# Optimization experiments

Measured on AMD Instinct MI355X. Metric: run time of the kernel, lower is better.

The kernel has to match this reference:

```python
import jax, jax.numpy as jnp
import numpy as np

T, B, DIN, DH, NH = 256, 256, 1024, 1024, 16
HD = DH // NH


def setup_inputs() -> dict:
    key = jax.random.key(0)
    ks = jax.random.split(key, 11)
    w = lambda k, shape: jax.random.normal(k, shape, jnp.float32) * 0.02
    return {
        "inputs": jax.random.normal(ks[0], (T, B, DIN), jnp.float32),
        "Wg": w(ks[1], (4, DIN + DH, DH)),  # forget, input, update, output pre-gate linears
        "bg": w(ks[2], (4, DH)),
        "Wq": w(ks[3], (3, DH, DH)),  # forget, input, output attention gates
        "bq": w(ks[4], (3, DH)),
        "Wk": w(ks[5], (3, DH, DH)),
        "bk": w(ks[6], (3, DH)),
        "Wv": w(ks[7], (3, DH, DH)),
        "bv": w(ks[8], (3, DH)),
        "Wo": w(ks[9], (3, DH, DH)),
        "bo": w(ks[10], (3, DH)),
    }


def reference(inputs, Wg, bg, Wq, bq, Wk, bk, Wv, bv, Wo, bo):
    scale = 1.0 / np.sqrt(HD)
    sel = jnp.array([0, 1, 3])  # gates that use attention: forget, input, output

    def attn_gate(x):
        # x: [3, B, DH] -- three gate pre-activations processed in parallel
        q = (jnp.einsum('gbd,gde->gbe', x, Wq) + bq[:, None, :]).reshape(3, B, NH, HD)
        k = (jnp.einsum('gbd,gde->gbe', x, Wk) + bk[:, None, :]).reshape(3, B, NH, HD)
        v = (jnp.einsum('gbd,gde->gbe', x, Wv) + bv[:, None, :]).reshape(3, B, NH, HD)
        # attention ACROSS heads: [3, B, NH, NH]
        aw = jax.nn.softmax(jnp.einsum('gbhd,gbkd->gbhk', q, k) * scale, axis=-1)
        ao = jnp.einsum('gbhk,gbkd->gbhd', aw, v).reshape(3, B, DH)
        return jax.nn.sigmoid(jnp.einsum('gbd,gde->gbe', ao, Wo) + bo[:, None, :])

    def step(carry, x):
        hx, cx = carry
        comb = jnp.concatenate([x, hx], axis=1)          # [B, DIN+DH]
        pre = jnp.einsum('bi,gio->gbo', comb, Wg) + bg[:, None, :]  # [4, B, DH]
        f, i, o = attn_gate(pre[sel])                    # each [B, DH]
        g = jnp.tanh(pre[2])
        cx = f * cx + i * g
        hx = o * jnp.tanh(cx)
        return (hx, cx), hx

    init = (jnp.zeros((B, DH), inputs.dtype), jnp.zeros((B, DH), inputs.dtype))
    (hx, cx), outputs = jax.lax.scan(step, init, inputs)
    return outputs, hx, cx
```

## Files before the change

kernel.cpp:

```cpp
#include <hip/hip_runtime.h>

typedef __attribute__((ext_vector_type(8))) short bf8;
typedef __attribute__((ext_vector_type(8))) unsigned short us8;
typedef __attribute__((ext_vector_type(4))) unsigned short us4;
typedef __attribute__((ext_vector_type(4))) float f4;

#define NB 256
#define OUT_HX_OFF ((size_t)256 * 256 * 1024)
#define OUT_CX_OFF (OUT_HX_OFF + (size_t)256 * 1024)

static __device__ __forceinline__ unsigned short f2bf(float f) {
    unsigned u = __builtin_bit_cast(unsigned, f);
    return (unsigned short)((u + 0x7FFFu + ((u >> 16) & 1u)) >> 16);
}
static __device__ __forceinline__ float bf2f(unsigned short h) {
    return __builtin_bit_cast(float, (unsigned)h << 16);
}
static __device__ __forceinline__ float sigm(float x) {
    return 1.0f / (1.0f + __expf(-x));
}

#define MFMA16(a, b, c) __builtin_amdgcn_mfma_f32_16x16x32_bf16(a, b, c, 0, 0, 0)

#define GLDS16(g, l)                                                        \
    __builtin_amdgcn_global_load_lds(                                       \
        (const __attribute__((address_space(1))) void*)(g),                 \
        (__attribute__((address_space(3))) void*)(l), 16, 0, 0)

#define WAITV(n) asm volatile("s_waitcnt vmcnt(" #n ")" ::: "memory")
#define WAITL0 asm volatile("s_waitcnt lgkmcnt(0)" ::: "memory")
#define BARRIER                                                             \
    do {                                                                    \
        __builtin_amdgcn_s_barrier();                                       \
        __builtin_amdgcn_sched_barrier(0);                                  \
    } while (0)

template <int R>
static __device__ __forceinline__ void stage64(const unsigned short* g, int gstride,
                                               unsigned short* lds, int wave, int lane) {
#pragma unroll
    for (int j = 0; j < R / 32; ++j) {
        const int seg = wave * (R / 32) + j;
        const int row = seg * 8 + (lane >> 3);
        const int chunk = (lane & 7) ^ (row & 7);
        GLDS16(g + (size_t)row * gstride + chunk * 8, lds + seg * 512);
    }
}

static __device__ __forceinline__ bf8 fragld(const unsigned short* lds, int row, int ck) {
    return *(const bf8*)&lds[row * 64 + (((ck) ^ (row & 7)) << 3)];
}

__global__ __launch_bounds__(256) void k_x2bf(const float* __restrict__ src,
                                              unsigned short* __restrict__ dst, int n4) {
    const int stride = gridDim.x * 256;
    for (int i = blockIdx.x * 256 + threadIdx.x; i < n4; i += stride) {
        f4 v = ((const f4*)src)[i];
        us4 o;
        o[0] = f2bf(v[0]); o[1] = f2bf(v[1]); o[2] = f2bf(v[2]); o[3] = f2bf(v[3]);
        ((us4*)dst)[i] = o;
    }
}

__global__ __launch_bounds__(256) void k_transpose(const float* __restrict__ src,
                                                   unsigned short* __restrict__ dst,
                                                   int K, int N) {
    __shared__ float tile[32][33];
    const int tx = threadIdx.x & 31, ty = threadIdx.x >> 5;
    const int n0 = blockIdx.x * 32, k0 = blockIdx.y * 32;
#pragma unroll
    for (int i = 0; i < 4; ++i) tile[ty + i * 8][tx] = src[(size_t)(k0 + ty + i * 8) * N + n0 + tx];
    __syncthreads();
#pragma unroll
    for (int i = 0; i < 4; ++i)
        dst[(size_t)(n0 + ty + i * 8) * K + k0 + tx] = f2bf(tile[tx][ty + i * 8]);
}

__global__ __launch_bounds__(256) void k_wf(const unsigned short* __restrict__ Aab,
                                            const unsigned short* __restrict__ Bb,
                                            unsigned short* __restrict__ outp,
                                            int outstride) {
    __shared__ unsigned short sA[2][128 * 64];
    __shared__ unsigned short sB[2][128 * 64];
    const int tid = threadIdx.x, lane = tid & 63, wave = tid >> 6;
    const int n0 = blockIdx.x * 128, m0 = blockIdx.y * 128;
    const int wy = (wave >> 1) * 64, wx = (wave & 1) * 64;
    const int fr = lane & 15, fq = lane >> 4;
    f4 acc[4][4] = {};

    stage64<128>(Aab + (size_t)m0 * 1024, 1024, sA[0], wave, lane);
    stage64<128>(Bb + (size_t)n0 * 1024, 1024, sB[0], wave, lane);
    WAITV(0); BARRIER;
#pragma unroll
    for (int i = 0; i < 16; ++i) {
        if (i + 1 < 16) {
            stage64<128>(Aab + (size_t)m0 * 1024 + (i + 1) * 64, 1024, sA[(i + 1) & 1], wave, lane);
            stage64<128>(Bb + (size_t)n0 * 1024 + (i + 1) * 64, 1024, sB[(i + 1) & 1], wave, lane);
        }
        const unsigned short* A = sA[i & 1];
        const unsigned short* Bm = sB[i & 1];
#pragma unroll
        for (int ks = 0; ks < 2; ++ks) {
            bf8 af[4], bfv[4];
#pragma unroll
            for (int mi = 0; mi < 4; ++mi) af[mi] = fragld(A, wy + mi * 16 + fr, ks * 4 + fq);
#pragma unroll
            for (int ni = 0; ni < 4; ++ni) bfv[ni] = fragld(Bm, wx + ni * 16 + fr, ks * 4 + fq);
#pragma unroll
            for (int mi = 0; mi < 4; ++mi)
#pragma unroll
                for (int ni = 0; ni < 4; ++ni)
                    acc[mi][ni] = MFMA16(af[mi], bfv[ni], acc[mi][ni]);
        }
        if (i + 1 < 16) { WAITL0; WAITV(0); BARRIER; }
    }
#pragma unroll
    for (int mi = 0; mi < 4; ++mi)
#pragma unroll
        for (int ni = 0; ni < 4; ++ni) {
            const int col = n0 + wx + ni * 16 + fr;
#pragma unroll
            for (int j = 0; j < 4; ++j) {
                const int row = m0 + wy + mi * 16 + fq * 4 + j;
                outp[(size_t)row * outstride + col] = f2bf(acc[mi][ni][j]);
            }
        }
}

__global__ __launch_bounds__(256) void k_seg9(const unsigned short* __restrict__ wgT,
                                              unsigned short* __restrict__ wbigX,
                                              unsigned short* __restrict__ wbigH) {
    const int d = blockIdx.x, k4 = threadIdx.x * 4;
    us4 vx = *(const us4*)(wgT + (size_t)(2048 + d) * 2048 + k4);
    us4 vh = *(const us4*)(wgT + (size_t)(2048 + d) * 2048 + 1024 + k4);
    *(us4*)(wbigX + (size_t)(9216 + d) * 1024 + k4) = vx;
    *(us4*)(wbigH + (size_t)(9216 + d) * 1024 + k4) = vh;
}

__global__ __launch_bounds__(256) void k_cbig(const float* __restrict__ bg,
                                              const float* __restrict__ Wq,
                                              const float* __restrict__ Wk,
                                              const float* __restrict__ Wv,
                                              const float* __restrict__ bq,
                                              const float* __restrict__ bk,
                                              const float* __restrict__ bv,
                                              float* __restrict__ cbig) {
    const int n = blockIdx.x * 256 + threadIdx.x;
    const int j = n >> 10, d = n & 1023;
    float s;
    if (j < 9) {
        const int gp = j / 3, which = j % 3;
        const int selg = (gp == 2) ? 3 : gp;
        const float* W = which == 0 ? Wq : (which == 1 ? Wk : Wv);
        const float* bqkv = which == 0 ? bq : (which == 1 ? bk : bv);
        s = bqkv[gp * 1024 + d];
        const float* wb = W + (size_t)gp * 1024 * 1024;
        const float* bgb = bg + selg * 1024;
        for (int k = 0; k < 1024; ++k) s += bgb[k] * wb[(size_t)k * 1024 + d];
    } else {
        s = bg[2048 + d];
    }
    cbig[n] = s;
}

__global__ __launch_bounds__(256) void k_xbig(const unsigned short* __restrict__ xbf,
                                              const unsigned short* __restrict__ wbigX,
                                              const float* __restrict__ cbig,
                                              unsigned short* __restrict__ XBIG) {
    __shared__ unsigned short sA[2][128 * 64];
    __shared__ unsigned short sB[2][128 * 64];
    const int tid = threadIdx.x, lane = tid & 63, wave = tid >> 6;
    const int n0 = blockIdx.x * 128;
    const size_t m0 = (size_t)blockIdx.y * 128;
    const int wy = (wave >> 1) * 64, wx = (wave & 1) * 64;
    const int fr = lane & 15, fq = lane >> 4;
    f4 acc[4][4] = {};

    stage64<128>(xbf + m0 * 1024, 1024, sA[0], wave, lane);
    stage64<128>(wbigX + (size_t)n0 * 1024, 1024, sB[0], wave, lane);
    WAITV(0); BARRIER;
#pragma unroll
    for (int i = 0; i < 16; ++i) {
        if (i + 1 < 16) {
            stage64<128>(xbf + m0 * 1024 + (i + 1) * 64, 1024, sA[(i + 1) & 1], wave, lane);
            stage64<128>(wbigX + (size_t)n0 * 1024 + (i + 1) * 64, 1024, sB[(i + 1) & 1], wave, lane);
        }
        const unsigned short* A = sA[i & 1];
        const unsigned short* Bm = sB[i & 1];
#pragma unroll
        for (int ks = 0; ks < 2; ++ks) {
            bf8 af[4], bfv[4];
#pragma unroll
            for (int mi = 0; mi < 4; ++mi) af[mi] = fragld(A, wy + mi * 16 + fr, ks * 4 + fq);
#pragma unroll
            for (int ni = 0; ni < 4; ++ni) bfv[ni] = fragld(Bm, wx + ni * 16 + fr, ks * 4 + fq);
#pragma unroll
            for (int mi = 0; mi < 4; ++mi)
#pragma unroll
                for (int ni = 0; ni < 4; ++ni)
                    acc[mi][ni] = MFMA16(af[mi], bfv[ni], acc[mi][ni]);
        }
        if (i + 1 < 16) { WAITL0; WAITV(0); BARRIER; }
    }
#pragma unroll
    for (int mi = 0; mi < 4; ++mi)
#pragma unroll
        for (int ni = 0; ni < 4; ++ni) {
            const int col = n0 + wx + ni * 16 + fr;
            const float b = cbig[col];
#pragma unroll
            for (int j = 0; j < 4; ++j) {
                const size_t row = m0 + wy + mi * 16 + fq * 4 + j;
                XBIG[row * 10240 + col] = f2bf(acc[mi][ni][j] + b);
            }
        }
}

__global__ __launch_bounds__(256) void k_xpre(const unsigned short* __restrict__ xbf,
                                              const unsigned short* __restrict__ wgT,
                                              const float* __restrict__ bg,
                                              unsigned short* __restrict__ xpre) {
    __shared__ unsigned short sA[2][128 * 64];
    __shared__ unsigned short sB[2][128 * 64];
    const int tid = threadIdx.x, lane = tid & 63, wave = tid >> 6;
    const int n0 = blockIdx.x * 128;
    const size_t m0 = (size_t)blockIdx.y * 128;
    const int wy = (wave >> 1) * 64, wx = (wave & 1) * 64;
    const int fr = lane & 15, fq = lane >> 4;
    f4 acc[4][4] = {};

    stage64<128>(xbf + m0 * 1024, 1024, sA[0], wave, lane);
    stage64<128>(wgT + (size_t)n0 * 2048, 2048, sB[0], wave, lane);
    WAITV(0); BARRIER;
#pragma unroll
    for (int i = 0; i < 16; ++i) {
        if (i + 1 < 16) {
            stage64<128>(xbf + m0 * 1024 + (i + 1) * 64, 1024, sA[(i + 1) & 1], wave, lane);
            stage64<128>(wgT + (size_t)n0 * 2048 + (i + 1) * 64, 2048, sB[(i + 1) & 1], wave, lane);
        }
        const unsigned short* A = sA[i & 1];
        const unsigned short* Bm = sB[i & 1];
#pragma unroll
        for (int ks = 0; ks < 2; ++ks) {
            bf8 af[4], bfv[4];
#pragma unroll
            for (int mi = 0; mi < 4; ++mi) af[mi] = fragld(A, wy + mi * 16 + fr, ks * 4 + fq);
#pragma unroll
            for (int ni = 0; ni < 4; ++ni) bfv[ni] = fragld(Bm, wx + ni * 16 + fr, ks * 4 + fq);
#pragma unroll
            for (int mi = 0; mi < 4; ++mi)
#pragma unroll
                for (int ni = 0; ni < 4; ++ni)
                    acc[mi][ni] = MFMA16(af[mi], bfv[ni], acc[mi][ni]);
        }
        if (i + 1 < 16) { WAITL0; WAITV(0); BARRIER; }
    }
#pragma unroll
    for (int mi = 0; mi < 4; ++mi)
#pragma unroll
        for (int ni = 0; ni < 4; ++ni) {
            const int col = n0 + wx + ni * 16 + fr;
            const float b = bg[col];
#pragma unroll
            for (int j = 0; j < 4; ++j) {
                const size_t row = m0 + wy + mi * 16 + fq * 4 + j;
                xpre[row * 4096 + col] = f2bf(acc[mi][ni][j] + b);
            }
        }
}

__global__ __launch_bounds__(256, 3) void k_qg(
    const unsigned short* __restrict__ hxbf,
    const unsigned short* __restrict__ wbigH,
    const unsigned short* __restrict__ XBIGt,
    unsigned short* __restrict__ qkvbf,
    float* __restrict__ gupd) {
    __shared__ unsigned short sA[4][32 * 64];
    __shared__ unsigned short sB[4][64 * 64];
    const int tid = threadIdx.x, lane = tid & 63, wave = tid >> 6;
    const int n0 = blockIdx.x * 64, b0 = blockIdx.y * 32;
    const unsigned short* Aab = hxbf + (size_t)b0 * 1024;
    const unsigned short* Bb = wbigH + (size_t)n0 * 1024;
    const int wr = (wave & 1) * 16, wc = (wave >> 1) * 32;
    const int fr = lane & 15, fq = lane >> 4;
    f4 acc[2] = {};

#pragma unroll
    for (int p = 0; p < 3; ++p) {
        stage64<32>(Aab + p * 64, 1024, sA[p], wave, lane);
        stage64<64>(Bb + p * 64, 1024, sB[p], wave, lane);
    }
    WAITV(6); BARRIER;
#pragma unroll
    for (int i = 0; i < 16; ++i) {
        if (i + 3 < 16) {
            stage64<32>(Aab + (i + 3) * 64, 1024, sA[(i + 3) & 3], wave, lane);
            stage64<64>(Bb + (i + 3) * 64, 1024, sB[(i + 3) & 3], wave, lane);
        }
        const unsigned short* A = sA[i & 3];
        const unsigned short* Bm = sB[i & 3];
#pragma unroll
        for (int ks = 0; ks < 2; ++ks) {
            bf8 a0 = fragld(A, wr + fr, ks * 4 + fq);
            bf8 b0v = fragld(Bm, wc + fr, ks * 4 + fq);
            bf8 b1v = fragld(Bm, wc + 16 + fr, ks * 4 + fq);
            acc[0] = MFMA16(a0, b0v, acc[0]);
            acc[1] = MFMA16(a0, b1v, acc[1]);
        }
        if (i < 15) {
            WAITL0;
            if (i + 3 < 16) { WAITV(6); }
            else if (i + 2 < 16) { WAITV(3); }
            else { WAITV(0); }
            BARRIER;
        }
    }
#pragma unroll
    for (int ni = 0; ni < 2; ++ni) {
        const int col = n0 + wc + ni * 16 + fr;
        const int seg = col >> 10, d = col & 1023;
#pragma unroll
        for (int j = 0; j < 4; ++j) {
            const int row = b0 + wr + fq * 4 + j;
            const float v = acc[ni][j] + bf2f(XBIGt[(size_t)row * 10240 + col]);
            if (seg == 9) {
                gupd[(size_t)row * 1024 + d] = tanhf(v);
            } else {
                const int gp = seg / 3, which = seg % 3;
                qkvbf[((size_t)gp * NB + row) * 3072 + which * 1024 + d] = f2bf(v);
            }
        }
    }
}

template <int XP>
__global__ __launch_bounds__(256, 2) void k_pre(
    const unsigned short* __restrict__ hxbf,
    const unsigned short* __restrict__ xt,
    const unsigned short* __restrict__ wgT,
    const float* __restrict__ bg,
    unsigned short* __restrict__ prebf,
    float* __restrict__ gupd) {
    __shared__ unsigned short sA[4][32 * 64];
    __shared__ unsigned short sB[4][64 * 64];
    const int tid = threadIdx.x, lane = tid & 63, wave = tid >> 6;
    const int n0 = blockIdx.x * 64, b0 = blockIdx.y * 32;
    const int wr = (wave & 1) * 16, wc = (wave >> 1) * 32;
    const int fr = lane & 15, fq = lane >> 4;
    constexpr int NT = XP ? 16 : 32;
    f4 acc[2] = {};

    const unsigned short* hb = hxbf + (size_t)b0 * 1024;
    const unsigned short* xb = xt + (XP ? 0 : (size_t)b0 * 1024);
    auto asrc = [&](int i) -> const unsigned short* {
        if (XP) return hb + i * 64;
        return i < 16 ? xb + i * 64 : hb + (i - 16) * 64;
    };
    auto bsrc = [&](int i) -> const unsigned short* {
        return wgT + (size_t)n0 * 2048 + (XP ? 1024 : 0) + i * 64;
    };

#pragma unroll
    for (int p = 0; p < 3; ++p) {
        stage64<32>(asrc(p), 1024, sA[p], wave, lane);
        stage64<64>(bsrc(p), 2048, sB[p], wave, lane);
    }
    WAITV(6); BARRIER;
#pragma unroll
    for (int i = 0; i < NT; ++i) {
        if (i + 3 < NT) {
            stage64<32>(asrc(i + 3), 1024, sA[(i + 3) & 3], wave, lane);
            stage64<64>(bsrc(i + 3), 2048, sB[(i + 3) & 3], wave, lane);
        }
        const unsigned short* A = sA[i & 3];
        const unsigned short* Bm = sB[i & 3];
#pragma unroll
        for (int ks = 0; ks < 2; ++ks) {
            bf8 a0 = fragld(A, wr + fr, ks * 4 + fq);
            bf8 b0v = fragld(Bm, wc + fr, ks * 4 + fq);
            bf8 b1v = fragld(Bm, wc + 16 + fr, ks * 4 + fq);
            acc[0] = MFMA16(a0, b0v, acc[0]);
            acc[1] = MFMA16(a0, b1v, acc[1]);
        }
        if (i < NT - 1) {
            WAITL0;
            if (i + 3 < NT) { WAITV(6); }
            else if (i + 2 < NT) { WAITV(3); }
            else { WAITV(0); }
            BARRIER;
        }
    }
#pragma unroll
    for (int ni = 0; ni < 2; ++ni) {
        const int col = n0 + wc + ni * 16 + fr;
        const int gg = col >> 10, d = col & 1023;
#pragma unroll
        for (int j = 0; j < 4; ++j) {
            const int row = b0 + wr + fq * 4 + j;
            float v = acc[ni][j];
            if (XP) v += bf2f(xt[(size_t)row * 4096 + col]);
            else v += bg[col];
            if (gg == 2) {
                gupd[(size_t)row * 1024 + d] = tanhf(v);
            } else {
                const int gm = (gg == 3) ? 2 : gg;
                prebf[((size_t)gm * NB + row) * 1024 + d] = f2bf(v);
            }
        }
    }
}

__global__ __launch_bounds__(256, 3) void k_qkv(
    const unsigned short* __restrict__ prebf,
    const unsigned short* __restrict__ wqkvT,
    const float* __restrict__ bq,
    const float* __restrict__ bk,
    const float* __restrict__ bv,
    unsigned short* __restrict__ qkvbf) {
    __shared__ unsigned short sA[4][32 * 64];
    __shared__ unsigned short sB[4][64 * 64];
    const int tid = threadIdx.x, lane = tid & 63, wave = tid >> 6;
    const int g = blockIdx.z;
    const int n0 = blockIdx.x * 64, b0 = blockIdx.y * 32;
    const unsigned short* Aab = prebf + ((size_t)g * NB + b0) * 1024;
    const unsigned short* Bb = wqkvT + ((size_t)g * 3072 + n0) * 1024;
    const int wr = (wave & 1) * 16, wc = (wave >> 1) * 32;
    const int fr = lane & 15, fq = lane >> 4;
    f4 acc[2] = {};

#pragma unroll
    for (int p = 0; p < 3; ++p) {
        stage64<32>(Aab + p * 64, 1024, sA[p], wave, lane);
        stage64<64>(Bb + p * 64, 1024, sB[p], wave, lane);
    }
    WAITV(6); BARRIER;
#pragma unroll
    for (int i = 0; i < 16; ++i) {
        if (i + 3 < 16) {
            stage64<32>(Aab + (i + 3) * 64, 1024, sA[(i + 3) & 3], wave, lane);
            stage64<64>(Bb + (i + 3) * 64, 1024, sB[(i + 3) & 3], wave, lane);
        }
        const unsigned short* A = sA[i & 3];
        const unsigned short* Bm = sB[i & 3];
#pragma unroll
        for (int ks = 0; ks < 2; ++ks) {
            bf8 a0 = fragld(A, wr + fr, ks * 4 + fq);
            bf8 b0v = fragld(Bm, wc + fr, ks * 4 + fq);
            bf8 b1v = fragld(Bm, wc + 16 + fr, ks * 4 + fq);
            acc[0] = MFMA16(a0, b0v, acc[0]);
            acc[1] = MFMA16(a0, b1v, acc[1]);
        }
        if (i < 15) {
            WAITL0;
            if (i + 3 < 16) { WAITV(6); }
            else if (i + 2 < 16) { WAITV(3); }
            else { WAITV(0); }
            BARRIER;
        }
    }
#pragma unroll
    for (int ni = 0; ni < 2; ++ni) {
        const int col = n0 + wc + ni * 16 + fr;
        const int which = col >> 10, d = col & 1023;
        const float* bp = which == 0 ? bq : (which == 1 ? bk : bv);
        const float bias = bp[g * 1024 + d];
#pragma unroll
        for (int j = 0; j < 4; ++j) {
            const int row = b0 + wr + fq * 4 + j;
            qkvbf[((size_t)g * NB + row) * 3072 + col] = f2bf(acc[ni][j] + bias);
        }
    }
}

__global__ __launch_bounds__(256) void k_attn(const unsigned short* __restrict__ qkvbf,
                                              unsigned short* __restrict__ aobf) {
    __shared__ unsigned short qs[16][72], ksm[16][72], vsm[16][72];
    __shared__ float aw[16][17];
    const int b = blockIdx.x, g = blockIdx.y, tid = threadIdx.x;
    const unsigned short* src = qkvbf + ((size_t)g * NB + b) * 3072;
#pragma unroll
    for (int j = 0; j < 3; ++j) {
        const int n = (j * 256 + tid) * 4;
        us4 dv = *(const us4*)(src + n);
        const int part = n >> 10, h = (n >> 6) & 15, c = n & 63;
        unsigned short* dst = part == 0 ? &qs[h][c] : (part == 1 ? &ksm[h][c] : &vsm[h][c]);
        *(us4*)dst = dv;
    }
    __syncthreads();
    const int h = tid >> 4, kp = tid & 15;
    float s = 0.f;
#pragma unroll
    for (int dblk = 0; dblk < 8; ++dblk) {
        us8 qv = *(const us8*)&qs[h][dblk * 8];
        us8 kv = *(const us8*)&ksm[kp][dblk * 8];
#pragma unroll
        for (int e = 0; e < 8; ++e) s += bf2f(qv[e]) * bf2f(kv[e]);
    }
    s *= 0.125f;
    float m = s;
#pragma unroll
    for (int off = 8; off; off >>= 1) m = fmaxf(m, __shfl_xor(m, off, 16));
    const float p = __expf(s - m);
    float sum = p;
#pragma unroll
    for (int off = 8; off; off >>= 1) sum += __shfl_xor(sum, off, 16);
    aw[h][kp] = p / sum;
    __syncthreads();
    float a0 = 0.f, a1 = 0.f, a2 = 0.f, a3 = 0.f;
#pragma unroll
    for (int kk = 0; kk < 16; ++kk) {
        const float w = aw[h][kk];
        us4 vv = *(const us4*)&vsm[kk][kp * 4];
        a0 += w * bf2f(vv[0]); a1 += w * bf2f(vv[1]);
        a2 += w * bf2f(vv[2]); a3 += w * bf2f(vv[3]);
    }
    us4 ov;
    ov[0] = f2bf(a0); ov[1] = f2bf(a1); ov[2] = f2bf(a2); ov[3] = f2bf(a3);
    *(us4*)(aobf + ((size_t)g * NB + b) * 1024 + h * 64 + kp * 4) = ov;
}

__global__ __launch_bounds__(256, 1) void k_gate(
    const unsigned short* __restrict__ aobf,
    const unsigned short* __restrict__ woT,
    const float* __restrict__ bo,
    const float* __restrict__ gupd,
    unsigned short* __restrict__ hxbf,
    float* __restrict__ out, int t) {
    __shared__ unsigned short sA[4][3][32 * 64];
    __shared__ unsigned short sB[4][3][32 * 64];
    const int tid = threadIdx.x, lane = tid & 63, wave = tid >> 6;
    const int d0 = blockIdx.x * 32, b0 = blockIdx.y * 32;
    const int wr = (wave & 1) * 16, wc = (wave >> 1) * 16;
    const int fr = lane & 15, fq = lane >> 4;
    f4 acc[3] = {};

    auto stage_all = [&](int i, int slot) {
#pragma unroll
        for (int g = 0; g < 3; ++g) {
            stage64<32>(aobf + ((size_t)g * NB + b0) * 1024 + i * 64, 1024,
                        sA[slot][g], wave, lane);
            stage64<32>(woT + ((size_t)g * 1024 + d0) * 1024 + i * 64, 1024,
                        sB[slot][g], wave, lane);
        }
    };

    stage_all(0, 0);
    stage_all(1, 1);
    stage_all(2, 2);
    WAITV(12); BARRIER;
#pragma unroll
    for (int i = 0; i < 16; ++i) {
        if (i + 3 < 16) stage_all(i + 3, (i + 3) & 3);
        const int sl = i & 3;
#pragma unroll
        for (int g = 0; g < 3; ++g) {
#pragma unroll
            for (int ks = 0; ks < 2; ++ks) {
                bf8 a0 = fragld(sA[sl][g], wr + fr, ks * 4 + fq);
                bf8 b0v = fragld(sB[sl][g], wc + fr, ks * 4 + fq);
                acc[g] = MFMA16(a0, b0v, acc[g]);
            }
        }
        if (i < 15) {
            WAITL0;
            if (i + 3 < 16) { WAITV(12); }
            else if (i + 2 < 16) { WAITV(6); }
            else { WAITV(0); }
            BARRIER;
        }
    }

    const int col = d0 + wc + fr;
    const float bof = bo[col], boi = bo[1024 + col], boo = bo[2048 + col];
    float* cxp = out + OUT_CX_OFF;
    float* hxp = out + OUT_HX_OFF;
    float* outs = out + (size_t)t * NB * 1024;
#pragma unroll
    for (int j = 0; j < 4; ++j) {
        const int row = b0 + wr + fq * 4 + j;
        const size_t idx = (size_t)row * 1024 + col;
        const float fg = sigm(acc[0][j] + bof);
        const float ig = sigm(acc[1][j] + boi);
        const float og = sigm(acc[2][j] + boo);
        const float c = fg * cxp[idx] + ig * gupd[idx];
        const float h = og * tanhf(c);
        cxp[idx] = c;
        hxp[idx] = h;
        outs[idx] = h;
        hxbf[idx] = f2bf(h);
    }
}

extern "C" void kernel_launch(void* const* d_in, const int* in_sizes, int n_in,
                              void* d_out, int out_size, void* d_ws, size_t ws_size,
                              hipStream_t stream) {
    const float* inputs = (const float*)d_in[0];
    const float* Wg = (const float*)d_in[1];
    const float* bg = (const float*)d_in[2];
    const float* Wq = (const float*)d_in[3];
    const float* bq = (const float*)d_in[4];
    const float* Wk = (const float*)d_in[5];
    const float* bk = (const float*)d_in[6];
    const float* Wv = (const float*)d_in[7];
    const float* bv = (const float*)d_in[8];
    const float* Wo = (const float*)d_in[9];
    const float* bo = (const float*)d_in[10];
    float* out = (float*)d_out;
    (void)in_sizes; (void)n_in; (void)out_size;

    char* ws = (char*)d_ws;
    size_t off = 0;
    auto alloc = [&](size_t bytes) -> void* {
        void* p = ws + off;
        off += (bytes + 255) & ~(size_t)255;
        return p;
    };
    unsigned short* wgT   = (unsigned short*)alloc((size_t)4096 * 2048 * 2);
    unsigned short* wqkvT = (unsigned short*)alloc((size_t)3 * 3072 * 1024 * 2);
    unsigned short* woT   = (unsigned short*)alloc((size_t)3 * 1024 * 1024 * 2);
    unsigned short* wgnt  = (unsigned short*)alloc((size_t)4 * 2048 * 1024 * 2);
    unsigned short* hxbf  = (unsigned short*)alloc((size_t)256 * 1024 * 2);
    unsigned short* prebf = (unsigned short*)alloc((size_t)3 * 256 * 1024 * 2);
    float*          gupd  = (float*)alloc((size_t)256 * 1024 * 4);
    unsigned short* qkvbf = (unsigned short*)alloc((size_t)3 * 256 * 3072 * 2);
    unsigned short* aobf  = (unsigned short*)alloc((size_t)3 * 256 * 1024 * 2);
    unsigned short* xbfs  = (unsigned short*)alloc((size_t)2 * 256 * 1024 * 2);
    const size_t off_base = off;
    unsigned short* xbf   = (unsigned short*)alloc((size_t)65536 * 1024 * 2);
    const size_t off_xbf = off;
    unsigned short* wbigX = (unsigned short*)alloc((size_t)10240 * 1024 * 2);
    unsigned short* wbigH = (unsigned short*)alloc((size_t)10240 * 1024 * 2);
    float*          cbig  = (float*)alloc((size_t)10240 * 4);
    unsigned short* XBIG  = (unsigned short*)alloc((size_t)65536 * 10240 * 2);
    const size_t off_tF = off;
    unsigned short* xpre  = wbigX;
    const size_t off_t1 = off_xbf + (((size_t)65536 * 4096 * 2 + 255) & ~(size_t)255);

    int tier;
    if (ws_size >= off_tF) tier = 0;
    else if (ws_size >= off_t1) tier = 1;
    else if (ws_size >= off_xbf) tier = 2;
    else if (ws_size >= off_base) tier = 3;
    else return;

    hipMemsetAsync(hxbf, 0, (size_t)256 * 1024 * 2, stream);
    hipMemsetAsync(out + OUT_CX_OFF, 0, (size_t)256 * 1024 * 4, stream);

    for (int g = 0; g < 4; ++g)
        k_transpose<<<dim3(32, 64), 256, 0, stream>>>(
            Wg + (size_t)g * 2048 * 1024, wgT + (size_t)g * 1024 * 2048, 2048, 1024);
    const float* wsrc[3] = {Wq, Wk, Wv};
    for (int g = 0; g < 3; ++g)
        for (int wi = 0; wi < 3; ++wi)
            k_transpose<<<dim3(32, 32), 256, 0, stream>>>(
                wsrc[wi] + (size_t)g * 1024 * 1024,
                wqkvT + (size_t)g * 3072 * 1024 + (size_t)wi * 1024 * 1024, 1024, 1024);
    for (int g = 0; g < 3; ++g)
        k_transpose<<<dim3(32, 32), 256, 0, stream>>>(
            Wo + (size_t)g * 1024 * 1024, woT + (size_t)g * 1024 * 1024, 1024, 1024);

    if (tier <= 2) k_x2bf<<<2048, 256, 0, stream>>>(inputs, xbf, 16777216);

    if (tier == 0) {
        k_x2bf<<<2048, 256, 0, stream>>>(Wg, wgnt, 2097152);
        for (int gp = 0; gp < 3; ++gp) {
            const int selg = (gp == 2) ? 3 : gp;
            for (int which = 0; which < 3; ++which) {
                const int j = gp * 3 + which;
                const unsigned short* A =
                    wqkvT + ((size_t)gp * 3072 + which * 1024) * 1024;
                const unsigned short* Bx = wgnt + (size_t)selg * 2048 * 1024;
                const unsigned short* Bh = Bx + (size_t)1024 * 1024;
                k_wf<<<dim3(8, 8), 256, 0, stream>>>(A, Bx, wbigX + (size_t)j * 1024 * 1024, 1024);
                k_wf<<<dim3(8, 8), 256, 0, stream>>>(A, Bh, wbigH + (size_t)j * 1024 * 1024, 1024);
            }
        }
        k_seg9<<<1024, 256, 0, stream>>>(wgT, wbigX, wbigH);
        k_cbig<<<40, 256, 0, stream>>>(bg, Wq, Wk, Wv, bq, bk, bv, cbig);
        k_xbig<<<dim3(80, 512), 256, 0, stream>>>(xbf, wbigX, cbig, XBIG);

        for (int t = 0; t < 256; ++t) {
            k_qg<<<dim3(160, 8), 256, 0, stream>>>(
                hxbf, wbigH, XBIG + (size_t)t * 256 * 10240, qkvbf, gupd);
            k_attn<<<dim3(256, 3), 256, 0, stream>>>(qkvbf, aobf);
            k_gate<<<dim3(32, 8), 256, 0, stream>>>(aobf, woT, bo, gupd, hxbf, out, t);
        }
    } else {
        if (tier == 1) k_xpre<<<dim3(32, 512), 256, 0, stream>>>(xbf, wgT, bg, xpre);
        for (int t = 0; t < 256; ++t) {
            if (tier == 3)
                k_x2bf<<<64, 256, 0, stream>>>(inputs + (size_t)t * 262144,
                                               xbfs + (size_t)(t & 1) * 262144, 65536);
            if (tier == 1)
                k_pre<1><<<dim3(64, 8), 256, 0, stream>>>(
                    hxbf, xpre + (size_t)t * 256 * 4096, wgT, bg, prebf, gupd);
            else
                k_pre<0><<<dim3(64, 8), 256, 0, stream>>>(
                    hxbf,
                    tier == 2 ? xbf + (size_t)t * 262144 : xbfs + (size_t)(t & 1) * 262144,
                    wgT, bg, prebf, gupd);
            k_qkv<<<dim3(48, 8, 3), 256, 0, stream>>>(prebf, wqkvT, bq, bk, bv, qkvbf);
            k_attn<<<dim3(256, 3), 256, 0, stream>>>(qkvbf, aobf);
            k_gate<<<dim3(32, 8), 256, 0, stream>>>(aobf, woT, bo, gupd, hxbf, out, t);
        }
    }
}
```

Baseline: 13.32 ms.

## Chunk the XBIG input projection by timestep and batch folded-weight GEMMs

```diff
diff --git a/kernel.cpp b/kernel.cpp
--- a/kernel.cpp
+++ b/kernel.cpp
@@ -76,13 +76,19 @@
         dst[(size_t)(n0 + ty + i * 8) * K + k0 + tx] = f2bf(tile[tx][ty + i * 8]);
 }
 
-__global__ __launch_bounds__(256) void k_wf(const unsigned short* __restrict__ Aab,
-                                            const unsigned short* __restrict__ Bb,
-                                            unsigned short* __restrict__ outp,
-                                            int outstride) {
+__global__ __launch_bounds__(256) void k_wfz(const unsigned short* __restrict__ wqkvT,
+                                             const unsigned short* __restrict__ wgnt,
+                                             unsigned short* __restrict__ wbigX,
+                                             unsigned short* __restrict__ wbigH) {
     __shared__ unsigned short sA[2][128 * 64];
     __shared__ unsigned short sB[2][128 * 64];
     const int tid = threadIdx.x, lane = tid & 63, wave = tid >> 6;
+    const int z = blockIdx.z, j = z >> 1, xh = z & 1;
+    const int gp = j / 3, which = j % 3;
+    const int selg = (gp == 2) ? 3 : gp;
+    const unsigned short* Aab = wqkvT + ((size_t)gp * 3072 + which * 1024) * 1024;
+    const unsigned short* Bb = wgnt + (size_t)selg * 2048 * 1024 + (size_t)xh * 1024 * 1024;
+    unsigned short* outp = (xh ? wbigH : wbigX) + (size_t)j * 1024 * 1024;
     const int n0 = blockIdx.x * 128, m0 = blockIdx.y * 128;
     const int wy = (wave >> 1) * 64, wx = (wave & 1) * 64;
     const int fr = lane & 15, fq = lane >> 4;
@@ -120,9 +126,9 @@
         for (int ni = 0; ni < 4; ++ni) {
             const int col = n0 + wx + ni * 16 + fr;
 #pragma unroll
-            for (int j = 0; j < 4; ++j) {
-                const int row = m0 + wy + mi * 16 + fq * 4 + j;
-                outp[(size_t)row * outstride + col] = f2bf(acc[mi][ni][j]);
+            for (int j2 = 0; j2 < 4; ++j2) {
+                const int row = m0 + wy + mi * 16 + fq * 4 + j2;
+                outp[(size_t)row * 1024 + col] = f2bf(acc[mi][ni][j2]);
             }
         }
 }
@@ -216,59 +222,6 @@
         }
 }
 
-__global__ __launch_bounds__(256) void k_xpre(const unsigned short* __restrict__ xbf,
-                                              const unsigned short* __restrict__ wgT,
-                                              const float* __restrict__ bg,
-                                              unsigned short* __restrict__ xpre) {
-    __shared__ unsigned short sA[2][128 * 64];
-    __shared__ unsigned short sB[2][128 * 64];
-    const int tid = threadIdx.x, lane = tid & 63, wave = tid >> 6;
-    const int n0 = blockIdx.x * 128;
-    const size_t m0 = (size_t)blockIdx.y * 128;
-    const int wy = (wave >> 1) * 64, wx = (wave & 1) * 64;
-    const int fr = lane & 15, fq = lane >> 4;
-    f4 acc[4][4] = {};
-
-    stage64<128>(xbf + m0 * 1024, 1024, sA[0], wave, lane);
-    stage64<128>(wgT + (size_t)n0 * 2048, 2048, sB[0], wave, lane);
-    WAITV(0); BARRIER;
-#pragma unroll
-    for (int i = 0; i < 16; ++i) {
-        if (i + 1 < 16) {
-            stage64<128>(xbf + m0 * 1024 + (i + 1) * 64, 1024, sA[(i + 1) & 1], wave, lane);
-            stage64<128>(wgT + (size_t)n0 * 2048 + (i + 1) * 64, 2048, sB[(i + 1) & 1], wave, lane);
-        }
-        const unsigned short* A = sA[i & 1];
-        const unsigned short* Bm = sB[i & 1];
-#pragma unroll
-        for (int ks = 0; ks < 2; ++ks) {
-            bf8 af[4], bfv[4];
-#pragma unroll
-            for (int mi = 0; mi < 4; ++mi) af[mi] = fragld(A, wy + mi * 16 + fr, ks * 4 + fq);
-#pragma unroll
-            for (int ni = 0; ni < 4; ++ni) bfv[ni] = fragld(Bm, wx + ni * 16 + fr, ks * 4 + fq);
-#pragma unroll
-            for (int mi = 0; mi < 4; ++mi)
-#pragma unroll
-                for (int ni = 0; ni < 4; ++ni)
-                    acc[mi][ni] = MFMA16(af[mi], bfv[ni], acc[mi][ni]);
-        }
-        if (i + 1 < 16) { WAITL0; WAITV(0); BARRIER; }
-    }
-#pragma unroll
-    for (int mi = 0; mi < 4; ++mi)
-#pragma unroll
-        for (int ni = 0; ni < 4; ++ni) {
-            const int col = n0 + wx + ni * 16 + fr;
-            const float b = bg[col];
-#pragma unroll
-            for (int j = 0; j < 4; ++j) {
-                const size_t row = m0 + wy + mi * 16 + fq * 4 + j;
-                xpre[row * 4096 + col] = f2bf(acc[mi][ni][j] + b);
-            }
-        }
-}
-
 __global__ __launch_bounds__(256, 3) void k_qg(
     const unsigned short* __restrict__ hxbf,
     const unsigned short* __restrict__ wbigH,
@@ -333,7 +286,6 @@
     }
 }
 
-template <int XP>
 __global__ __launch_bounds__(256, 2) void k_pre(
     const unsigned short* __restrict__ hxbf,
     const unsigned short* __restrict__ xt,
@@ -347,17 +299,16 @@
     const int n0 = blockIdx.x * 64, b0 = blockIdx.y * 32;
     const int wr = (wave & 1) * 16, wc = (wave >> 1) * 32;
     const int fr = lane & 15, fq = lane >> 4;
-    constexpr int NT = XP ? 16 : 32;
+    constexpr int NT = 32;
     f4 acc[2] = {};
 
     const unsigned short* hb = hxbf + (size_t)b0 * 1024;
-    const unsigned short* xb = xt + (XP ? 0 : (size_t)b0 * 1024);
+    const unsigned short* xb = xt + (size_t)b0 * 1024;
     auto asrc = [&](int i) -> const unsigned short* {
-        if (XP) return hb + i * 64;
         return i < 16 ? xb + i * 64 : hb + (i - 16) * 64;
     };
     auto bsrc = [&](int i) -> const unsigned short* {
-        return wgT + (size_t)n0 * 2048 + (XP ? 1024 : 0) + i * 64;
+        return wgT + (size_t)n0 * 2048 + i * 64;
     };
 
 #pragma unroll
@@ -397,9 +348,7 @@
 #pragma unroll
         for (int j = 0; j < 4; ++j) {
             const int row = b0 + wr + fq * 4 + j;
-            float v = acc[ni][j];
-            if (XP) v += bf2f(xt[(size_t)row * 4096 + col]);
-            else v += bg[col];
+            float v = acc[ni][j] + bg[col];
             if (gg == 2) {
                 gupd[(size_t)row * 1024 + d] = tanhf(v);
             } else {
@@ -631,14 +580,15 @@
     unsigned short* wbigX = (unsigned short*)alloc((size_t)10240 * 1024 * 2);
     unsigned short* wbigH = (unsigned short*)alloc((size_t)10240 * 1024 * 2);
     float*          cbig  = (float*)alloc((size_t)10240 * 4);
-    unsigned short* XBIG  = (unsigned short*)alloc((size_t)65536 * 10240 * 2);
-    const size_t off_tF = off;
-    unsigned short* xpre  = wbigX;
-    const size_t off_t1 = off_xbf + (((size_t)65536 * 4096 * 2 + 255) & ~(size_t)255);
-
+    const size_t off_wb = off;
+    unsigned short* XBIGc = (unsigned short*)(ws + off_wb);
+
+    int CH = 0;
+    for (int c = 64; c >= 4; c >>= 1) {
+        if (ws_size >= off_wb + (size_t)c * 256 * 10240 * 2) { CH = c; break; }
+    }
     int tier;
-    if (ws_size >= off_tF) tier = 0;
-    else if (ws_size >= off_t1) tier = 1;
+    if (CH > 0) tier = 0;
     else if (ws_size >= off_xbf) tier = 2;
     else if (ws_size >= off_base) tier = 3;
     else return;
@@ -663,42 +613,30 @@
 
     if (tier == 0) {
         k_x2bf<<<2048, 256, 0, stream>>>(Wg, wgnt, 2097152);
-        for (int gp = 0; gp < 3; ++gp) {
-            const int selg = (gp == 2) ? 3 : gp;
-            for (int which = 0; which < 3; ++which) {
-                const int j = gp * 3 + which;
-                const unsigned short* A =
-                    wqkvT + ((size_t)gp * 3072 + which * 1024) * 1024;
-                const unsigned short* Bx = wgnt + (size_t)selg * 2048 * 1024;
-                const unsigned short* Bh = Bx + (size_t)1024 * 1024;
-                k_wf<<<dim3(8, 8), 256, 0, stream>>>(A, Bx, wbigX + (size_t)j * 1024 * 1024, 1024);
-                k_wf<<<dim3(8, 8), 256, 0, stream>>>(A, Bh, wbigH + (size_t)j * 1024 * 1024, 1024);
-            }
-        }
+        k_wfz<<<dim3(8, 8, 18), 256, 0, stream>>>(wqkvT, wgnt, wbigX, wbigH);
         k_seg9<<<1024, 256, 0, stream>>>(wgT, wbigX, wbigH);
         k_cbig<<<40, 256, 0, stream>>>(bg, Wq, Wk, Wv, bq, bk, bv, cbig);
-        k_xbig<<<dim3(80, 512), 256, 0, stream>>>(xbf, wbigX, cbig, XBIG);
-
-        for (int t = 0; t < 256; ++t) {
-            k_qg<<<dim3(160, 8), 256, 0, stream>>>(
-                hxbf, wbigH, XBIG + (size_t)t * 256 * 10240, qkvbf, gupd);
-            k_attn<<<dim3(256, 3), 256, 0, stream>>>(qkvbf, aobf);
-            k_gate<<<dim3(32, 8), 256, 0, stream>>>(aobf, woT, bo, gupd, hxbf, out, t);
+
+        for (int c = 0; c < 256 / CH; ++c) {
+            k_xbig<<<dim3(80, CH * 2), 256, 0, stream>>>(
+                xbf + (size_t)c * CH * 256 * 1024, wbigX, cbig, XBIGc);
+            for (int tl = 0; tl < CH; ++tl) {
+                const int t = c * CH + tl;
+                k_qg<<<dim3(160, 8), 256, 0, stream>>>(
+                    hxbf, wbigH, XBIGc + (size_t)tl * 256 * 10240, qkvbf, gupd);
+                k_attn<<<dim3(256, 3), 256, 0, stream>>>(qkvbf, aobf);
+                k_gate<<<dim3(32, 8), 256, 0, stream>>>(aobf, woT, bo, gupd, hxbf, out, t);
+            }
         }
     } else {
-        if (tier == 1) k_xpre<<<dim3(32, 512), 256, 0, stream>>>(xbf, wgT, bg, xpre);
         for (int t = 0; t < 256; ++t) {
             if (tier == 3)
                 k_x2bf<<<64, 256, 0, stream>>>(inputs + (size_t)t * 262144,
                                                xbfs + (size_t)(t & 1) * 262144, 65536);
-            if (tier == 1)
-                k_pre<1><<<dim3(64, 8), 256, 0, stream>>>(
-                    hxbf, xpre + (size_t)t * 256 * 4096, wgT, bg, prebf, gupd);
-            else
-                k_pre<0><<<dim3(64, 8), 256, 0, stream>>>(
-                    hxbf,
-                    tier == 2 ? xbf + (size_t)t * 262144 : xbfs + (size_t)(t & 1) * 262144,
-                    wgT, bg, prebf, gupd);
+            k_pre<<<dim3(64, 8), 256, 0, stream>>>(
+                hxbf,
+                tier == 2 ? xbf + (size_t)t * 262144 : xbfs + (size_t)(t & 1) * 262144,
+                wgT, bg, prebf, gupd);
             k_qkv<<<dim3(48, 8, 3), 256, 0, stream>>>(prebf, wqkvT, bq, bk, bv, qkvbf);
             k_attn<<<dim3(256, 3), 256, 0, stream>>>(qkvbf, aobf);
             k_gate<<<dim3(32, 8), 256, 0, stream>>>(aobf, woT, bo, gupd, hxbf, out, t);
```

Result: faster. 12.89 ms (median of 2 runs) (-3.2%).
